# Kernel optimization log

Measured on AMD Instinct MI355X. Metric: run time of the kernel, lower is better.

## Reference

```python
import jax, jax.numpy as jnp
import numpy as np

ATOM_FEAT_DIM = 32
HIDDEN = 512
N = 4096


def _linear_params(key, in_dim, out_dim):
    kw, kb = jax.random.split(key)
    bound = 1.0 / np.sqrt(in_dim)
    W = jax.random.uniform(kw, (out_dim, in_dim), minval=-bound, maxval=bound, dtype=jnp.float32)
    b = jax.random.uniform(kb, (out_dim,), minval=-bound, maxval=bound, dtype=jnp.float32)
    return W, b


def setup_inputs() -> dict:
    key = jax.random.key(0)
    ks = jax.random.split(key, 8)
    x = jax.random.normal(ks[0], (N, ATOM_FEAT_DIM), dtype=jnp.float32)
    adj = jax.random.uniform(ks[1], (N, N), dtype=jnp.float32)
    w_self1, b_self1 = _linear_params(ks[2], ATOM_FEAT_DIM, HIDDEN)
    w_neigh1, b_neigh1 = _linear_params(ks[3], ATOM_FEAT_DIM, HIDDEN)
    w_self2, b_self2 = _linear_params(ks[4], HIDDEN, HIDDEN)
    w_neigh2, b_neigh2 = _linear_params(ks[5], HIDDEN, HIDDEN)
    w_atom, b_atom = _linear_params(ks[6], HIDDEN, ATOM_FEAT_DIM)
    w_bond, b_bond = _linear_params(ks[7], 2 * HIDDEN, 4)
    return dict(x=x, adj=adj,
                w_self1=w_self1, b_self1=b_self1, w_neigh1=w_neigh1, b_neigh1=b_neigh1,
                w_self2=w_self2, b_self2=b_self2, w_neigh2=w_neigh2, b_neigh2=b_neigh2,
                w_atom=w_atom, b_atom=b_atom, w_bond=w_bond, b_bond=b_bond)


def _graph_conv(x, adj, w_self, b_self, w_neigh, b_neigh):
    deg = jnp.clip(adj.sum(axis=-1, keepdims=True), 1.0, None)  # (N,1)
    agg = (adj @ x) / deg
    return jax.nn.relu(x @ w_self.T + b_self + agg @ w_neigh.T + b_neigh)


def reference(x, adj, w_self1, b_self1, w_neigh1, b_neigh1,
              w_self2, b_self2, w_neigh2, b_neigh2,
              w_atom, b_atom, w_bond, b_bond):
    h1 = _graph_conv(x, adj, w_self1, b_self1, w_neigh1, b_neigh1)
    h2 = _graph_conv(h1, adj, w_self2, b_self2, w_neigh2, b_neigh2)  # (N,H)
    atom_logits = h2 @ w_atom.T + b_atom  # (N,F)
    # bond_head(cat(h2[i],h2[j])) = h2[i]@W[:, :H].T + h2[j]@W[:, H:].T + b
    H = h2.shape[1]
    a = h2 @ w_bond[:, :H].T  # (N,4) contribution of node i
    b = h2 @ w_bond[:, H:].T  # (N,4) contribution of node j
    upper = a[:, None, :] + b[None, :, :] + b_bond  # logits for pair (i,j)
    n = h2.shape[0]
    iu = jnp.triu(jnp.ones((n, n), dtype=h2.dtype), k=1)[:, :, None]  # i<j mask
    # original fills bond[i,j]=bond[j,i]=logits(i,j) for i<j; diagonal stays zero
    bond_logits = upper * iu + jnp.swapaxes(upper, 0, 1) * jnp.swapaxes(iu, 0, 1)
    return atom_logits, bond_logits
```

## Files before the change

### kernel.cpp

```cpp
#include <hip/hip_runtime.h>

#define N_ATOMS 4096
#define FDIM 32
#define HID 512

typedef __bf16 bf16x8 __attribute__((ext_vector_type(8)));
typedef float f32x4 __attribute__((ext_vector_type(4)));

__device__ __forceinline__ float bf2f(ushort h) {
  union { uint u; float f; } v; v.u = ((uint)h) << 16; return v.f;
}
__device__ __forceinline__ ushort f2bf(float f) {
  union { float f; uint u; } v; v.f = f;
  uint u = v.u;
  u += 0x7fffu + ((u >> 16) & 1u);
  return (ushort)(u >> 16);
}

__device__ __forceinline__ void gload16(const ushort* g, ushort* l) {
  __builtin_amdgcn_global_load_lds(
      (const __attribute__((address_space(1))) void*)g,
      (__attribute__((address_space(3))) void*)l,
      16, 0, 0);
}

__global__ __launch_bounds__(256) void prep_adj(const float* __restrict__ adj,
                                                ushort* __restrict__ adjb,
                                                float* __restrict__ rdeg) {
  const int row = blockIdx.x;
  const int t = threadIdx.x;
  const float* r = adj + (size_t)row * N_ATOMS;
  ushort* w = adjb + (size_t)row * N_ATOMS;
  float s = 0.f;
#pragma unroll
  for (int i = 0; i < 4; i++) {
    const int c = (t + i * 256) * 4;
    float4 v = *(const float4*)(r + c);
    s += v.x + v.y + v.z + v.w;
    ushort4 o;
    o.x = f2bf(v.x); o.y = f2bf(v.y); o.z = f2bf(v.z); o.w = f2bf(v.w);
    *(ushort4*)(w + c) = o;
  }
#pragma unroll
  for (int off = 32; off; off >>= 1) s += __shfl_down(s, off);
  __shared__ float red[4];
  if ((t & 63) == 0) red[t >> 6] = s;
  __syncthreads();
  if (t == 0) rdeg[row] = 1.f / fmaxf(red[0] + red[1] + red[2] + red[3], 1.f);
}

__global__ __launch_bounds__(256) void prep_x(const float* __restrict__ x,
                                              ushort* __restrict__ xt) {
  const int idx = blockIdx.x * 256 + threadIdx.x;
  const int m = idx >> 5, c = idx & 31;
  xt[(size_t)c * N_ATOMS + m] = f2bf(x[(size_t)m * FDIM + c]);
}

__global__ __launch_bounds__(256) void prep_w2(const float* __restrict__ ws2,
                                               const float* __restrict__ wn2,
                                               ushort* __restrict__ wcat2) {
  const int idx = blockIdx.x * 256 + threadIdx.x;
  const int n = idx >> 10, k = idx & 1023;
  float v = (k < 512) ? ws2[(size_t)n * 512 + k] : wn2[(size_t)n * 512 + k - 512];
  wcat2[idx] = f2bf(v);
}

template<int BM, int BN, int WROWS, int WCOLS>
__global__ __launch_bounds__(256, 2) void gemm_nt(
    const ushort* __restrict__ A, int lda,
    const ushort* __restrict__ B, int ldb,
    int Kchunk, float* __restrict__ Cout, int ldc)
{
  constexpr int WTM = BM / WROWS;
  constexpr int WTN = BN / WCOLS;
  constexpr int MT = WTM / 16;
  constexpr int NT = WTN / 16;
  constexpr int AL = BM / 32;
  constexpr int BL = BN / 32;

  __shared__ __align__(16) ushort As[BM * 64];
  __shared__ __align__(16) ushort Bs[BN * 64];

  const int t = threadIdx.x;
  const int wave = t >> 6;
  const int lane = t & 63;
  const int q = lane >> 4;
  const int ln = lane & 15;
  const int wr = wave / WCOLS;
  const int wc = wave % WCOLS;
  const int mbase = wr * WTM;
  const int nbase = wc * WTN;

  const int n0 = blockIdx.x * BN;
  const int m0 = blockIdx.y * BM;
  const int kbase = blockIdx.z * Kchunk;

  f32x4 acc[MT][NT];
#pragma unroll
  for (int i = 0; i < MT; i++)
#pragma unroll
    for (int j = 0; j < NT; j++)
#pragma unroll
      for (int r = 0; r < 4; r++) acc[i][j][r] = 0.f;

  for (int kt = 0; kt < Kchunk; kt += 64) {
    const int kg = kbase + kt;
#pragma unroll
    for (int i = 0; i < AL; i++) {
      const int g = (wave * AL + i) * 64 + lane;
      const int row = g >> 3, c8 = g & 7;
      gload16(A + (size_t)(m0 + row) * lda + kg + c8 * 8, &As[g * 8]);
    }
#pragma unroll
    for (int i = 0; i < BL; i++) {
      const int g = (wave * BL + i) * 64 + lane;
      const int row = g >> 3, c8 = g & 7;
      gload16(B + (size_t)(n0 + row) * ldb + kg + c8 * 8, &Bs[g * 8]);
    }
    __syncthreads();
#pragma unroll
    for (int kk = 0; kk < 64; kk += 32) {
      bf16x8 af[MT], bfr[NT];
#pragma unroll
      for (int i = 0; i < MT; i++)
        af[i] = *(const bf16x8*)(&As[(mbase + i * 16 + ln) * 64 + kk + q * 8]);
#pragma unroll
      for (int j = 0; j < NT; j++)
        bfr[j] = *(const bf16x8*)(&Bs[(nbase + j * 16 + ln) * 64 + kk + q * 8]);
#pragma unroll
      for (int i = 0; i < MT; i++)
#pragma unroll
        for (int j = 0; j < NT; j++)
          acc[i][j] = __builtin_amdgcn_mfma_f32_16x16x32_bf16(af[i], bfr[j], acc[i][j], 0, 0, 0);
    }
    __syncthreads();
  }

#pragma unroll
  for (int i = 0; i < MT; i++)
#pragma unroll
    for (int j = 0; j < NT; j++)
#pragma unroll
      for (int r = 0; r < 4; r++) {
        const int m = m0 + mbase + i * 16 + q * 4 + r;
        const int n = n0 + nbase + j * 16 + ln;
        atomicAdd(Cout + (size_t)m * ldc + n, acc[i][j][r]);
      }
}

__global__ __launch_bounds__(256) void epi_agg2(const float* __restrict__ gf,
                                                const float* __restrict__ rdeg,
                                                ushort* __restrict__ cat2) {
  const int idx = blockIdx.x * 256 + threadIdx.x;
  const int m = idx >> 7;
  const int n4 = (idx & 127) * 4;
  const float r = rdeg[m];
  float4 v = *(const float4*)(gf + (size_t)m * HID + n4);
  ushort4 o;
  o.x = f2bf(v.x * r); o.y = f2bf(v.y * r);
  o.z = f2bf(v.z * r); o.w = f2bf(v.w * r);
  *(ushort4*)(cat2 + (size_t)m * 1024 + 512 + n4) = o;
}

__global__ __launch_bounds__(256) void h1_kernel(
    const float* __restrict__ x, const float* __restrict__ agg1,
    const float* __restrict__ rdeg,
    const float* __restrict__ ws1, const float* __restrict__ bs1,
    const float* __restrict__ wn1, const float* __restrict__ bn1,
    ushort* __restrict__ cat2, ushort* __restrict__ h1t)
{
  const int idx = blockIdx.x * 256 + threadIdx.x;
  const int m = idx >> 9;
  const int n = idx & 511;
  const float* xr = x + (size_t)m * FDIM;
  const float* ar = agg1 + (size_t)m * FDIM;
  const float* w1 = ws1 + (size_t)n * FDIM;
  const float* w2 = wn1 + (size_t)n * FDIM;
  float accs = 0.f, accn = 0.f;
#pragma unroll
  for (int k = 0; k < FDIM; k += 4) {
    float4 xv = *(const float4*)(xr + k);
    float4 av = *(const float4*)(ar + k);
    float4 wv = *(const float4*)(w1 + k);
    float4 nv = *(const float4*)(w2 + k);
    accs += xv.x * wv.x + xv.y * wv.y + xv.z * wv.z + xv.w * wv.w;
    accn += av.x * nv.x + av.y * nv.y + av.z * nv.z + av.w * nv.w;
  }
  float v = fmaxf(accs + accn * rdeg[m] + bs1[n] + bn1[n], 0.f);
  ushort h = f2bf(v);
  cat2[(size_t)m * 1024 + n] = h;
  h1t[(size_t)n * N_ATOMS + m] = h;
}

__global__ __launch_bounds__(256) void heads_kernel(
    const float* __restrict__ h2f,
    const float* __restrict__ bs2, const float* __restrict__ bn2,
    const float* __restrict__ w_atom, const float* __restrict__ b_atom,
    const float* __restrict__ w_bond,
    float* __restrict__ atom_out,
    float* __restrict__ a_buf, float* __restrict__ b_buf)
{
  const int idx = blockIdx.x * 256 + threadIdx.x;
  if (idx >= N_ATOMS * 40) return;
  const int m = idx / 40;
  const int c = idx - m * 40;
  const float* hr = h2f + (size_t)m * HID;
  const float* wr;
  if (c < 32)      wr = w_atom + (size_t)c * HID;
  else if (c < 36) wr = w_bond + (size_t)(c - 32) * 1024;
  else             wr = w_bond + (size_t)(c - 36) * 1024 + 512;
  float acc = 0.f;
#pragma unroll 4
  for (int k = 0; k < HID; k += 4) {
    float4 hv = *(const float4*)(hr + k);
    float4 s0 = *(const float4*)(bs2 + k);
    float4 s1 = *(const float4*)(bn2 + k);
    float4 w0 = *(const float4*)(wr + k);
    acc += fmaxf(hv.x + s0.x + s1.x, 0.f) * w0.x
         + fmaxf(hv.y + s0.y + s1.y, 0.f) * w0.y
         + fmaxf(hv.z + s0.z + s1.z, 0.f) * w0.z
         + fmaxf(hv.w + s0.w + s1.w, 0.f) * w0.w;
  }
  if (c < 32)      atom_out[(size_t)m * 32 + c] = acc + b_atom[c];
  else if (c < 36) a_buf[(size_t)m * 4 + (c - 32)] = acc;
  else             b_buf[(size_t)m * 4 + (c - 36)] = acc;
}

__global__ __launch_bounds__(256) void bond_fill(
    const float* __restrict__ av, const float* __restrict__ bv,
    const float* __restrict__ bbond, float* __restrict__ out)
{
  const int idx = blockIdx.x * 256 + threadIdx.x;
  const int i = idx >> 12;
  const int j = idx & 4095;
  float4 r;
  if (i < j) {
    float4 ai = *(const float4*)(av + (size_t)i * 4);
    float4 bj = *(const float4*)(bv + (size_t)j * 4);
    r.x = ai.x + bj.x + bbond[0]; r.y = ai.y + bj.y + bbond[1];
    r.z = ai.z + bj.z + bbond[2]; r.w = ai.w + bj.w + bbond[3];
  } else if (i > j) {
    float4 aj = *(const float4*)(av + (size_t)j * 4);
    float4 bi = *(const float4*)(bv + (size_t)i * 4);
    r.x = aj.x + bi.x + bbond[0]; r.y = aj.y + bi.y + bbond[1];
    r.z = aj.z + bi.z + bbond[2]; r.w = aj.w + bi.w + bbond[3];
  } else {
    r.x = r.y = r.z = r.w = 0.f;
  }
  *(float4*)(out + (size_t)idx * 4) = r;
}

extern "C" void kernel_launch(void* const* d_in, const int* in_sizes, int n_in,
                              void* d_out, int out_size, void* d_ws, size_t ws_size,
                              hipStream_t stream)
{
  const float* x        = (const float*)d_in[0];
  const float* adj      = (const float*)d_in[1];
  const float* w_self1  = (const float*)d_in[2];
  const float* b_self1  = (const float*)d_in[3];
  const float* w_neigh1 = (const float*)d_in[4];
  const float* b_neigh1 = (const float*)d_in[5];
  const float* w_self2  = (const float*)d_in[6];
  const float* b_self2  = (const float*)d_in[7];
  const float* w_neigh2 = (const float*)d_in[8];
  const float* b_neigh2 = (const float*)d_in[9];
  const float* w_atom   = (const float*)d_in[10];
  const float* b_atom   = (const float*)d_in[11];
  const float* w_bond   = (const float*)d_in[12];
  const float* b_bond   = (const float*)d_in[13];

  char* w = (char*)d_ws;
  float*  rdeg  = (float*)w;  w += (size_t)N_ATOMS * sizeof(float);
  float*  agg1  = (float*)w;  w += (size_t)N_ATOMS * FDIM * sizeof(float);
  float*  a_buf = (float*)w;  w += (size_t)N_ATOMS * 4 * sizeof(float);
  float*  b_buf = (float*)w;  w += (size_t)N_ATOMS * 4 * sizeof(float);
  ushort* adjb  = (ushort*)w; w += (size_t)N_ATOMS * N_ATOMS * sizeof(ushort);
  ushort* xt    = (ushort*)w; w += (size_t)FDIM * N_ATOMS * sizeof(ushort);
  ushort* h1t   = (ushort*)w; w += (size_t)HID * N_ATOMS * sizeof(ushort);
  ushort* cat2  = (ushort*)w; w += (size_t)N_ATOMS * 1024 * sizeof(ushort);
  ushort* wcat2 = (ushort*)w; w += (size_t)HID * 1024 * sizeof(ushort);
  float*  gf    = (float*)w;  w += (size_t)N_ATOMS * HID * sizeof(float);

  float* atom_out = (float*)d_out;
  float* bond_out = (float*)d_out + (size_t)N_ATOMS * FDIM;

  prep_adj<<<N_ATOMS, 256, 0, stream>>>(adj, adjb, rdeg);
  prep_x<<<(N_ATOMS * FDIM) / 256, 256, 0, stream>>>(x, xt);
  prep_w2<<<(HID * 1024) / 256, 256, 0, stream>>>(w_self2, w_neigh2, wcat2);
  hipMemsetAsync(agg1, 0, (size_t)N_ATOMS * FDIM * sizeof(float), stream);
  hipMemsetAsync(gf, 0, (size_t)N_ATOMS * HID * sizeof(float), stream);

  gemm_nt<128, 32, 4, 1><<<dim3(1, 32, 16), 256, 0, stream>>>(
      adjb, N_ATOMS, xt, N_ATOMS, 256, agg1, FDIM);
  h1_kernel<<<(N_ATOMS * HID) / 256, 256, 0, stream>>>(
      x, agg1, rdeg, w_self1, b_self1, w_neigh1, b_neigh1, cat2, h1t);
  gemm_nt<128, 128, 2, 2><<<dim3(4, 32, 4), 256, 0, stream>>>(
      adjb, N_ATOMS, h1t, N_ATOMS, 1024, gf, HID);
  epi_agg2<<<(N_ATOMS * HID / 4) / 256, 256, 0, stream>>>(gf, rdeg, cat2);
  hipMemsetAsync(gf, 0, (size_t)N_ATOMS * HID * sizeof(float), stream);
  gemm_nt<128, 128, 2, 2><<<dim3(4, 32, 4), 256, 0, stream>>>(
      cat2, 1024, wcat2, 1024, 256, gf, HID);
  heads_kernel<<<(N_ATOMS * 40 + 255) / 256, 256, 0, stream>>>(
      gf, b_self2, b_neigh2, w_atom, b_atom, w_bond, atom_out, a_buf, b_buf);
  bond_fill<<<(N_ATOMS * N_ATOMS) / 256, 256, 0, stream>>>(a_buf, b_buf, b_bond, bond_out);
}
```

Baseline: 593.2 us.

## Replace split-K atomicAdd with per-slice stores and separate reduction kernels

The split-K GEMMs now write their partial results into separate slice buffers with plain stores instead of atomicAdd into one zeroed buffer. Dedicated reduction kernels (red_agg1, epi_agg2, and a new epi_h2) sum the slices and apply the epilogue, which removes the memsets and atomic contention. Bias plus ReLU for h2 is now done once in epi_h2 rather than inside every heads_kernel dot product. The bond bias is folded into a_buf so bond_fill no longer adds it. In exchange the code uses a larger workspace and reads and writes more traffic through the slice buffers.

```diff
diff --git a/kernel.cpp b/kernel.cpp
--- a/kernel.cpp
+++ b/kernel.cpp
@@ -69,7 +69,7 @@
 __global__ __launch_bounds__(256, 2) void gemm_nt(
     const ushort* __restrict__ A, int lda,
     const ushort* __restrict__ B, int ldb,
-    int Kchunk, float* __restrict__ Cout, int ldc)
+    int Kchunk, float* __restrict__ Cout, int ldc, size_t cstride)
 {
   constexpr int WTM = BM / WROWS;
   constexpr int WTN = BN / WCOLS;
@@ -94,6 +94,7 @@
   const int n0 = blockIdx.x * BN;
   const int m0 = blockIdx.y * BM;
   const int kbase = blockIdx.z * Kchunk;
+  float* __restrict__ Cs = Cout + (size_t)blockIdx.z * cstride;
 
   f32x4 acc[MT][NT];
 #pragma unroll
@@ -144,22 +145,62 @@
       for (int r = 0; r < 4; r++) {
         const int m = m0 + mbase + i * 16 + q * 4 + r;
         const int n = n0 + nbase + j * 16 + ln;
-        atomicAdd(Cout + (size_t)m * ldc + n, acc[i][j][r]);
+        Cs[(size_t)m * ldc + n] = acc[i][j][r];
       }
 }
 
-__global__ __launch_bounds__(256) void epi_agg2(const float* __restrict__ gf,
+__global__ __launch_bounds__(256) void red_agg1(const float* __restrict__ sl,
+                                                float* __restrict__ agg1) {
+  const int idx = blockIdx.x * 256 + threadIdx.x;
+  f32x4 s = {0.f, 0.f, 0.f, 0.f};
+#pragma unroll
+  for (int z = 0; z < 16; z++) {
+    f32x4 v = *(const f32x4*)(sl + (size_t)z * N_ATOMS * FDIM + (size_t)idx * 4);
+    s += v;
+  }
+  *(f32x4*)(agg1 + (size_t)idx * 4) = s;
+}
+
+__global__ __launch_bounds__(256) void epi_agg2(const float* __restrict__ sl,
                                                 const float* __restrict__ rdeg,
                                                 ushort* __restrict__ cat2) {
   const int idx = blockIdx.x * 256 + threadIdx.x;
   const int m = idx >> 7;
   const int n4 = (idx & 127) * 4;
+  f32x4 s = {0.f, 0.f, 0.f, 0.f};
+#pragma unroll
+  for (int z = 0; z < 4; z++) {
+    f32x4 v = *(const f32x4*)(sl + (size_t)z * N_ATOMS * HID + (size_t)m * HID + n4);
+    s += v;
+  }
   const float r = rdeg[m];
-  float4 v = *(const float4*)(gf + (size_t)m * HID + n4);
   ushort4 o;
-  o.x = f2bf(v.x * r); o.y = f2bf(v.y * r);
-  o.z = f2bf(v.z * r); o.w = f2bf(v.w * r);
+  o.x = f2bf(s[0] * r); o.y = f2bf(s[1] * r);
+  o.z = f2bf(s[2] * r); o.w = f2bf(s[3] * r);
   *(ushort4*)(cat2 + (size_t)m * 1024 + 512 + n4) = o;
+}
+
+__global__ __launch_bounds__(256) void epi_h2(const float* __restrict__ sl,
+                                              const float* __restrict__ bs2,
+                                              const float* __restrict__ bn2,
+                                              float* __restrict__ h2f) {
+  const int idx = blockIdx.x * 256 + threadIdx.x;
+  const int m = idx >> 7;
+  const int n4 = (idx & 127) * 4;
+  f32x4 s = {0.f, 0.f, 0.f, 0.f};
+#pragma unroll
+  for (int z = 0; z < 4; z++) {
+    f32x4 v = *(const f32x4*)(sl + (size_t)z * N_ATOMS * HID + (size_t)m * HID + n4);
+    s += v;
+  }
+  float4 b0 = *(const float4*)(bs2 + n4);
+  float4 b1 = *(const float4*)(bn2 + n4);
+  f32x4 o;
+  o[0] = fmaxf(s[0] + b0.x + b1.x, 0.f);
+  o[1] = fmaxf(s[1] + b0.y + b1.y, 0.f);
+  o[2] = fmaxf(s[2] + b0.z + b1.z, 0.f);
+  o[3] = fmaxf(s[3] + b0.w + b1.w, 0.f);
+  *(f32x4*)(h2f + (size_t)m * HID + n4) = o;
 }
 
 __global__ __launch_bounds__(256) void h1_kernel(
@@ -194,9 +235,8 @@
 
 __global__ __launch_bounds__(256) void heads_kernel(
     const float* __restrict__ h2f,
-    const float* __restrict__ bs2, const float* __restrict__ bn2,
     const float* __restrict__ w_atom, const float* __restrict__ b_atom,
-    const float* __restrict__ w_bond,
+    const float* __restrict__ w_bond, const float* __restrict__ b_bond,
     float* __restrict__ atom_out,
     float* __restrict__ a_buf, float* __restrict__ b_buf)
 {
@@ -213,22 +253,17 @@
 #pragma unroll 4
   for (int k = 0; k < HID; k += 4) {
     float4 hv = *(const float4*)(hr + k);
-    float4 s0 = *(const float4*)(bs2 + k);
-    float4 s1 = *(const float4*)(bn2 + k);
     float4 w0 = *(const float4*)(wr + k);
-    acc += fmaxf(hv.x + s0.x + s1.x, 0.f) * w0.x
-         + fmaxf(hv.y + s0.y + s1.y, 0.f) * w0.y
-         + fmaxf(hv.z + s0.z + s1.z, 0.f) * w0.z
-         + fmaxf(hv.w + s0.w + s1.w, 0.f) * w0.w;
+    acc += hv.x * w0.x + hv.y * w0.y + hv.z * w0.z + hv.w * w0.w;
   }
   if (c < 32)      atom_out[(size_t)m * 32 + c] = acc + b_atom[c];
-  else if (c < 36) a_buf[(size_t)m * 4 + (c - 32)] = acc;
+  else if (c < 36) a_buf[(size_t)m * 4 + (c - 32)] = acc + b_bond[c - 32];
   else             b_buf[(size_t)m * 4 + (c - 36)] = acc;
 }
 
 __global__ __launch_bounds__(256) void bond_fill(
     const float* __restrict__ av, const float* __restrict__ bv,
-    const float* __restrict__ bbond, float* __restrict__ out)
+    float* __restrict__ out)
 {
   const int idx = blockIdx.x * 256 + threadIdx.x;
   const int i = idx >> 12;
@@ -237,13 +272,13 @@
   if (i < j) {
     float4 ai = *(const float4*)(av + (size_t)i * 4);
     float4 bj = *(const float4*)(bv + (size_t)j * 4);
-    r.x = ai.x + bj.x + bbond[0]; r.y = ai.y + bj.y + bbond[1];
-    r.z = ai.z + bj.z + bbond[2]; r.w = ai.w + bj.w + bbond[3];
+    r.x = ai.x + bj.x; r.y = ai.y + bj.y;
+    r.z = ai.z + bj.z; r.w = ai.w + bj.w;
   } else if (i > j) {
     float4 aj = *(const float4*)(av + (size_t)j * 4);
     float4 bi = *(const float4*)(bv + (size_t)i * 4);
-    r.x = aj.x + bi.x + bbond[0]; r.y = aj.y + bi.y + bbond[1];
-    r.z = aj.z + bi.z + bbond[2]; r.w = aj.w + bi.w + bbond[3];
+    r.x = aj.x + bi.x; r.y = aj.y + bi.y;
+    r.z = aj.z + bi.z; r.w = aj.w + bi.w;
   } else {
     r.x = r.y = r.z = r.w = 0.f;
   }
@@ -279,7 +314,8 @@
   ushort* h1t   = (ushort*)w; w += (size_t)HID * N_ATOMS * sizeof(ushort);
   ushort* cat2  = (ushort*)w; w += (size_t)N_ATOMS * 1024 * sizeof(ushort);
   ushort* wcat2 = (ushort*)w; w += (size_t)HID * 1024 * sizeof(ushort);
-  float*  gf    = (float*)w;  w += (size_t)N_ATOMS * HID * sizeof(float);
+  float*  h2f   = (float*)w;  w += (size_t)N_ATOMS * HID * sizeof(float);
+  float*  sl    = (float*)w;  w += (size_t)4 * N_ATOMS * HID * sizeof(float);
 
   float* atom_out = (float*)d_out;
   float* bond_out = (float*)d_out + (size_t)N_ATOMS * FDIM;
@@ -287,20 +323,19 @@
   prep_adj<<<N_ATOMS, 256, 0, stream>>>(adj, adjb, rdeg);
   prep_x<<<(N_ATOMS * FDIM) / 256, 256, 0, stream>>>(x, xt);
   prep_w2<<<(HID * 1024) / 256, 256, 0, stream>>>(w_self2, w_neigh2, wcat2);
-  hipMemsetAsync(agg1, 0, (size_t)N_ATOMS * FDIM * sizeof(float), stream);
-  hipMemsetAsync(gf, 0, (size_t)N_ATOMS * HID * sizeof(float), stream);
 
   gemm_nt<128, 32, 4, 1><<<dim3(1, 32, 16), 256, 0, stream>>>(
-      adjb, N_ATOMS, xt, N_ATOMS, 256, agg1, FDIM);
+      adjb, N_ATOMS, xt, N_ATOMS, 256, sl, FDIM, (size_t)N_ATOMS * FDIM);
+  red_agg1<<<(N_ATOMS * FDIM / 4) / 256, 256, 0, stream>>>(sl, agg1);
   h1_kernel<<<(N_ATOMS * HID) / 256, 256, 0, stream>>>(
       x, agg1, rdeg, w_self1, b_self1, w_neigh1, b_neigh1, cat2, h1t);
   gemm_nt<128, 128, 2, 2><<<dim3(4, 32, 4), 256, 0, stream>>>(
-      adjb, N_ATOMS, h1t, N_ATOMS, 1024, gf, HID);
-  epi_agg2<<<(N_ATOMS * HID / 4) / 256, 256, 0, stream>>>(gf, rdeg, cat2);
-  hipMemsetAsync(gf, 0, (size_t)N_ATOMS * HID * sizeof(float), stream);
+      adjb, N_ATOMS, h1t, N_ATOMS, 1024, sl, HID, (size_t)N_ATOMS * HID);
+  epi_agg2<<<(N_ATOMS * HID / 4) / 256, 256, 0, stream>>>(sl, rdeg, cat2);
   gemm_nt<128, 128, 2, 2><<<dim3(4, 32, 4), 256, 0, stream>>>(
-      cat2, 1024, wcat2, 1024, 256, gf, HID);
+      cat2, 1024, wcat2, 1024, 256, sl, HID, (size_t)N_ATOMS * HID);
+  epi_h2<<<(N_ATOMS * HID / 4) / 256, 256, 0, stream>>>(sl, b_self2, b_neigh2, h2f);
   heads_kernel<<<(N_ATOMS * 40 + 255) / 256, 256, 0, stream>>>(
-      gf, b_self2, b_neigh2, w_atom, b_atom, w_bond, atom_out, a_buf, b_buf);
-  bond_fill<<<(N_ATOMS * N_ATOMS) / 256, 256, 0, stream>>>(a_buf, b_buf, b_bond, bond_out);
-}
+      h2f, w_atom, b_atom, w_bond, b_bond, atom_out, a_buf, b_buf);
+  bond_fill<<<(N_ATOMS * N_ATOMS) / 256, 256, 0, stream>>>(a_buf, b_buf, bond_out);
+}
```

After: 557.6 us. 6.0% less time.
